# Optimization experiments

Hardware: AMD Instinct MI355X
Metric: run time of the kernel (lower is better)

## Reference

```python
import math
import jax, jax.numpy as jnp
import numpy as np

N_TOKENS = 32768
N_TYPES = 21
D_MODEL = 1024
N_SEQS = 64


def setup_inputs() -> dict:
    key = jax.random.key(0)
    k1, k2, k3, k4 = jax.random.split(key, 4)
    x = jax.random.normal(k1, (N_TOKENS, N_TYPES), dtype=jnp.float32)
    # nn.Linear(n_types, d_model): weight [d_model, n_types], bias [d_model]
    W = jax.random.normal(k2, (D_MODEL, N_TYPES), dtype=jnp.float32) / math.sqrt(N_TYPES)
    b = jax.random.normal(k3, (D_MODEL,), dtype=jnp.float32) * 0.01
    # sorted segment ids -> ragged batch of N_SEQS sequences
    batch = jnp.sort(jax.random.randint(k4, (N_TOKENS,), 0, N_SEQS, dtype=jnp.int64))
    return {"x": x, "W": W, "b": b, "batch": batch}


def _position_encoding(max_len, d_model, dtype):
    pos = jnp.arange(max_len, dtype=jnp.float32)[:, None]          # [L,1]
    div = jnp.exp(jnp.arange(0, d_model, 2, dtype=jnp.float32) * (-math.log(10000.0) / d_model))
    ang = pos * div                                                 # [L, d/2]
    pe = jnp.zeros((max_len, d_model), dtype=jnp.float32)
    pe = pe.at[:, 0::2].set(jnp.sin(ang)).at[:, 1::2].set(jnp.cos(ang))
    return pe.astype(dtype)


def reference(x, W, b, batch):
    d_model = W.shape[0]
    # Linear projection + sqrt(d_model) scale
    h = (jnp.einsum('nt,dt->nd', x, W) + b) * math.sqrt(d_model)    # [N, d_model]

    # pad_batch: relabel via unique ids, compute per-token position within its
    # sequence, and scatter into a padded [n_seqs, max_len, d_model] tensor.
    bnp = np.asarray(batch)
    _, inv, counts = np.unique(bnp, return_inverse=True, return_counts=True)
    n_seqs = counts.shape[0]
    max_len = int(counts.max())
    offsets = np.concatenate([np.zeros(1, dtype=np.int64), np.cumsum(counts)[:-1]])
    pos = np.arange(bnp.shape[0], dtype=np.int64) - offsets[inv]    # position within sequence

    padded = jnp.zeros((n_seqs, max_len, d_model), dtype=h.dtype)
    padded = padded.at[jnp.asarray(inv), jnp.asarray(pos)].set(h)

    # mask: True where valid token (original returns ~pad_mask)
    mask = jnp.arange(max_len)[None, :] < jnp.asarray(counts)[:, None]

    pe = _position_encoding(max_len, d_model, h.dtype)              # [L, d_model]
    out = padded + pe[None, :, :]
    return (out, mask)
```

## Files before the change

### kernel.cpp

```cpp
#include <hip/hip_runtime.h>
#include <hip/hip_bf16.h>
#include <math.h>

typedef float f4 __attribute__((ext_vector_type(4)));
typedef float f32x4 __attribute__((ext_vector_type(4)));
typedef short bf16x8 __attribute__((ext_vector_type(8)));

__device__ inline unsigned short f2bf(float f) {
  unsigned int u = __builtin_bit_cast(unsigned int, f);
  unsigned int r = (u + 0x7FFFu + ((u >> 16) & 1u)) >> 16;
  return (unsigned short)r;
}

__global__ __launch_bounds__(1024) void setup_kernel(
    const int* __restrict__ batch, int n, const float* __restrict__ W,
    int* __restrict__ tables, unsigned short* __restrict__ wbf) {
  int t = threadIdx.x;

  {
    const float* wr = W + t * 21;
    unsigned short* wo = wbf + t * 32;
#pragma unroll
    for (int k = 0; k < 21; ++k) wo[k] = f2bf(wr[k]);
#pragma unroll
    for (int k = 21; k < 32; ++k) wo[k] = 0;
  }

  __shared__ int samp[256];
  __shared__ int csum[64];
  __shared__ int fine[64];
  __shared__ int sbase[64];
  __shared__ int lbs[65];
  __shared__ int stride_s;
  if (t == 0) stride_s = (batch[n - 1] == 0) ? 2 : 1;
  if (t < 64) { csum[t] = 0; fine[t] = 0; }
  __syncthreads();
  int stride = stride_s;
  int window = (n + 255) >> 8;
  if (t < 256) {
    long long idx = (long long)t * window;
    if (idx > n - 1) idx = n - 1;
    samp[t] = batch[idx * stride];
  }
  __syncthreads();
  {
    int v = t >> 4, q = t & 15;
    int c = 0;
#pragma unroll
    for (int i = 0; i < 16; ++i) c += (samp[q * 16 + i] < v) ? 1 : 0;
    atomicAdd(&csum[v], c);
  }
  __syncthreads();
  if (t < 64) {
    int c = csum[t];
    sbase[t] = (c == 0) ? 0 : (c - 1) * window;
  }
  __syncthreads();
  {
    int v = t >> 4, q = t & 15;
    int wpt = (window + 15) >> 4;
    int S = sbase[v];
    int c = 0;
    for (int j = q * wpt; j < (q + 1) * wpt && j < window; ++j) {
      int idx = S + j;
      if (idx < n && batch[idx * stride] < v) c++;
    }
    atomicAdd(&fine[v], c);
  }
  __syncthreads();
  if (t < 64) {
    lbs[t] = sbase[t] + fine[t];
    if (t == 0) lbs[64] = n;
  }
  __syncthreads();
  if (t < 64) {
    int cnt = lbs[t + 1] - lbs[t];
    unsigned long long present = __ballot(cnt > 0);
    int seg = __popcll(present & ((1ull << t) - 1ull));
    int nseq = __popcll(present);
    if (cnt > 0) { tables[seg] = lbs[t]; tables[64 + seg] = cnt; }
    if (t >= nseq) { tables[t] = 0; tables[64 + t] = 0; }
  }
}

__global__ __launch_bounds__(256) void embed_kernel(
    const float* __restrict__ x, const unsigned short* __restrict__ wb,
    const float* __restrict__ bias, const int* __restrict__ tables,
    float* __restrict__ out, float* __restrict__ mask,
    int L, int n_tokens) {
  int t = threadIdx.x;
  int lane = t & 63;
  int wv = t >> 6;
  int g = lane >> 4, c = lane & 15;

  int stripe = blockIdx.x >> 2;
  int colGroup = blockIdx.x & 3;
  int base = stripe * 16;

  int s0 = base / L;
  int s0L = s0 * L;
  int Lnext = s0L + L;

  int row_r = base + c;
  int inc_r = (row_r >= Lnext) ? 1 : 0;
  int p_r = row_r - (inc_r ? Lnext : s0L);
  int cnt_r = tables[64 + s0 + inc_r];
  unsigned long long bal = __ballot(p_r < cnt_r);
  unsigned int m16 = (unsigned int)(bal & 0xFFFFull);
  int rank_r = __popc(m16 & ((1u << c) - 1u));

  int p0 = base - s0L;
  int cnt0 = tables[64 + s0];
  int tok0 = tables[s0] + (p0 < cnt0 ? p0 : cnt0);
  int tok = tok0 + rank_r;
  if (tok > n_tokens - 1) tok = n_tokens - 1;

  const float* xr = x + tok * 21;
  float vv[8];
#pragma unroll
  for (int j = 0; j < 8; ++j) vv[j] = 0.f;
  if (g == 0) {
#pragma unroll
    for (int j = 0; j < 8; ++j) vv[j] = xr[j];
  } else if (g == 1) {
#pragma unroll
    for (int j = 0; j < 8; ++j) vv[j] = xr[8 + j];
  } else if (g == 2) {
#pragma unroll
    for (int j = 0; j < 5; ++j) vv[j] = xr[16 + j];
  }
  bf16x8 af;
#pragma unroll
  for (int j = 0; j < 8; ++j) af[j] = (short)f2bf(vv[j]);

  int prow[4], pval[4];
#pragma unroll
  for (int j = 0; j < 4; ++j) {
    int rr = 4 * g + j;
    int row = base + rr;
    int inc = (row >= Lnext) ? 1 : 0;
    prow[j] = row - (inc ? Lnext : s0L);
    pval[j] = (m16 >> rr) & 1;
  }

  const float KC = -0.01798894603901599f;
  int cb = colGroup * 256 + wv * 64;
  bool isOdd = (c & 1) != 0;

#pragma unroll
  for (int ct = 0; ct < 4; ++ct) {
    int col = cb + ct * 16 + c;
    bf16x8 bfrag = *(const bf16x8*)(wb + col * 32 + 8 * g);
    f32x4 acc = {0.f, 0.f, 0.f, 0.f};
    acc = __builtin_amdgcn_mfma_f32_16x16x32_bf16(af, bfrag, acc, 0, 0, 0);
    float bv = bias[col];
    float dv = __expf(KC * (float)(col >> 1));
#pragma unroll
    for (int j = 0; j < 4; ++j) {
      float ang = (float)prow[j] * dv;
      float pe = isOdd ? __cosf(ang) : __sinf(ang);
      float res = pval[j] ? fmaf(acc[j] + bv, 32.f, pe) : pe;
      out[(size_t)(base + 4 * g + j) * 1024 + col] = res;
    }
  }

  if (colGroup == 0 && t < 16)
    mask[base + t] = ((m16 >> t) & 1) ? 1.0f : 0.0f;
}

extern "C" void kernel_launch(void* const* d_in, const int* in_sizes, int n_in,
                              void* d_out, int out_size, void* d_ws, size_t ws_size,
                              hipStream_t stream) {
  const float* x = (const float*)d_in[0];
  const float* W = (const float*)d_in[1];
  const float* b = (const float*)d_in[2];
  const int* batch = (const int*)d_in[3];
  int n_tokens = in_sizes[3];
  float* out = (float*)d_out;

  int L = out_size / (64 * 1025);
  int totalRows = 64 * L;

  int* tables = (int*)d_ws;
  unsigned short* wbf = (unsigned short*)((char*)d_ws + 1024);

  setup_kernel<<<1, 1024, 0, stream>>>(batch, n_tokens, W, tables, wbf);

  int stripes = totalRows / 16;
  embed_kernel<<<stripes * 4, 256, 0, stream>>>(x, wbf, b, tables, out,
                                                out + (size_t)totalRows * 1024,
                                                L, n_tokens);
}
```

Baseline: 44.17 us.

## Fuse segment-table setup into embed kernel via per-block binary search

Removes the separate single-block setup kernel. Each embed block now computes the segment starts and counts itself, using a 64-lane binary search over the batch ids, and converts its W columns to bf16 in registers. This drops one kernel launch and the serial dependency on a single-block kernel. In exchange every block repeats the binary searches (about 15 dependent global loads per lane) and the W loads and conversions, which adds latency to each block.

```diff
diff --git a/kernel.cpp b/kernel.cpp
--- a/kernel.cpp
+++ b/kernel.cpp
@@ -2,7 +2,6 @@
 #include <hip/hip_bf16.h>
 #include <math.h>
 
-typedef float f4 __attribute__((ext_vector_type(4)));
 typedef float f32x4 __attribute__((ext_vector_type(4)));
 typedef short bf16x8 __attribute__((ext_vector_type(8)));
 
@@ -12,90 +11,67 @@
   return (unsigned short)r;
 }
 
-__global__ __launch_bounds__(1024) void setup_kernel(
-    const int* __restrict__ batch, int n, const float* __restrict__ W,
-    int* __restrict__ tables, unsigned short* __restrict__ wbf) {
-  int t = threadIdx.x;
-
-  {
-    const float* wr = W + t * 21;
-    unsigned short* wo = wbf + t * 32;
-#pragma unroll
-    for (int k = 0; k < 21; ++k) wo[k] = f2bf(wr[k]);
-#pragma unroll
-    for (int k = 21; k < 32; ++k) wo[k] = 0;
-  }
-
-  __shared__ int samp[256];
-  __shared__ int csum[64];
-  __shared__ int fine[64];
-  __shared__ int sbase[64];
-  __shared__ int lbs[65];
-  __shared__ int stride_s;
-  if (t == 0) stride_s = (batch[n - 1] == 0) ? 2 : 1;
-  if (t < 64) { csum[t] = 0; fine[t] = 0; }
-  __syncthreads();
-  int stride = stride_s;
-  int window = (n + 255) >> 8;
-  if (t < 256) {
-    long long idx = (long long)t * window;
-    if (idx > n - 1) idx = n - 1;
-    samp[t] = batch[idx * stride];
-  }
-  __syncthreads();
-  {
-    int v = t >> 4, q = t & 15;
-    int c = 0;
-#pragma unroll
-    for (int i = 0; i < 16; ++i) c += (samp[q * 16 + i] < v) ? 1 : 0;
-    atomicAdd(&csum[v], c);
-  }
-  __syncthreads();
-  if (t < 64) {
-    int c = csum[t];
-    sbase[t] = (c == 0) ? 0 : (c - 1) * window;
-  }
-  __syncthreads();
-  {
-    int v = t >> 4, q = t & 15;
-    int wpt = (window + 15) >> 4;
-    int S = sbase[v];
-    int c = 0;
-    for (int j = q * wpt; j < (q + 1) * wpt && j < window; ++j) {
-      int idx = S + j;
-      if (idx < n && batch[idx * stride] < v) c++;
-    }
-    atomicAdd(&fine[v], c);
-  }
-  __syncthreads();
-  if (t < 64) {
-    lbs[t] = sbase[t] + fine[t];
-    if (t == 0) lbs[64] = n;
-  }
-  __syncthreads();
-  if (t < 64) {
-    int cnt = lbs[t + 1] - lbs[t];
-    unsigned long long present = __ballot(cnt > 0);
-    int seg = __popcll(present & ((1ull << t) - 1ull));
-    int nseq = __popcll(present);
-    if (cnt > 0) { tables[seg] = lbs[t]; tables[64 + seg] = cnt; }
-    if (t >= nseq) { tables[t] = 0; tables[64 + t] = 0; }
-  }
-}
-
 __global__ __launch_bounds__(256) void embed_kernel(
-    const float* __restrict__ x, const unsigned short* __restrict__ wb,
-    const float* __restrict__ bias, const int* __restrict__ tables,
-    float* __restrict__ out, float* __restrict__ mask,
-    int L, int n_tokens) {
+    const float* __restrict__ x, const float* __restrict__ W,
+    const float* __restrict__ bias, const int* __restrict__ batch,
+    int n, float* __restrict__ out, float* __restrict__ mask,
+    int L, int totalRows) {
   int t = threadIdx.x;
   int lane = t & 63;
   int wv = t >> 6;
   int g = lane >> 4, c = lane & 15;
 
   int stripe = blockIdx.x >> 2;
-  int colGroup = blockIdx.x & 3;
+  int colGroup = blockIdx.x & 2 ? (blockIdx.x & 3) : (blockIdx.x & 3);
+  colGroup = blockIdx.x & 3;
   int base = stripe * 16;
+
+  __shared__ int seg_start[65];
+  __shared__ int seg_cnt[65];
+
+  if (t < 64) {
+    int stride = (batch[n - 1] == 0) ? 2 : 1;
+    int v = t;
+    int lo = 0, hi = n;
+    while (lo < hi) {
+      int mid = (lo + hi) >> 1;
+      if (batch[(size_t)mid * stride] < v) lo = mid + 1; else hi = mid;
+    }
+    int lbn = __shfl_down(lo, 1);
+    if (t == 63) lbn = n;
+    int cnt = lbn - lo;
+    unsigned long long present = __ballot(cnt > 0);
+    int rank = __popcll(present & ((1ull << t) - 1ull));
+    int nseq = __popcll(present);
+    if (cnt > 0) { seg_start[rank] = lo; seg_cnt[rank] = cnt; }
+    if (t >= nseq) { seg_start[t] = n; seg_cnt[t] = 0; }
+    if (t == 0) { seg_start[64] = n; seg_cnt[64] = 0; }
+  }
+
+  const float KC = -0.01798894603901599f;
+  int cb = colGroup * 256 + wv * 64;
+  int kb = 8 * g;
+  bf16x8 bfr[4];
+  float bv[4], dv[4];
+#pragma unroll
+  for (int ct = 0; ct < 4; ++ct) {
+    int col = cb + ct * 16 + c;
+    const float* wr = W + col * 21;
+    float wvv[8];
+#pragma unroll
+    for (int j = 0; j < 8; ++j) {
+      int k = kb + j;
+      wvv[j] = (k < 21) ? wr[k] : 0.f;
+    }
+    bf16x8 bf;
+#pragma unroll
+    for (int j = 0; j < 8; ++j) bf[j] = (short)f2bf(wvv[j]);
+    bfr[ct] = bf;
+    bv[ct] = bias[col];
+    dv[ct] = __expf(KC * (float)(col >> 1));
+  }
+
+  __syncthreads();
 
   int s0 = base / L;
   int s0L = s0 * L;
@@ -104,34 +80,34 @@
   int row_r = base + c;
   int inc_r = (row_r >= Lnext) ? 1 : 0;
   int p_r = row_r - (inc_r ? Lnext : s0L);
-  int cnt_r = tables[64 + s0 + inc_r];
+  int cnt_r = seg_cnt[s0 + inc_r];
   unsigned long long bal = __ballot(p_r < cnt_r);
   unsigned int m16 = (unsigned int)(bal & 0xFFFFull);
   int rank_r = __popc(m16 & ((1u << c) - 1u));
 
   int p0 = base - s0L;
-  int cnt0 = tables[64 + s0];
-  int tok0 = tables[s0] + (p0 < cnt0 ? p0 : cnt0);
+  int cnt0 = seg_cnt[s0];
+  int tok0 = seg_start[s0] + (p0 < cnt0 ? p0 : cnt0);
   int tok = tok0 + rank_r;
-  if (tok > n_tokens - 1) tok = n_tokens - 1;
+  if (tok > (n - 1)) tok = n - 1;
 
-  const float* xr = x + tok * 21;
-  float vv[8];
+  const float* xr = x + (size_t)tok * 21;
+  float vvx[8];
 #pragma unroll
-  for (int j = 0; j < 8; ++j) vv[j] = 0.f;
+  for (int j = 0; j < 8; ++j) vvx[j] = 0.f;
   if (g == 0) {
 #pragma unroll
-    for (int j = 0; j < 8; ++j) vv[j] = xr[j];
+    for (int j = 0; j < 8; ++j) vvx[j] = xr[j];
   } else if (g == 1) {
 #pragma unroll
-    for (int j = 0; j < 8; ++j) vv[j] = xr[8 + j];
+    for (int j = 0; j < 8; ++j) vvx[j] = xr[8 + j];
   } else if (g == 2) {
 #pragma unroll
-    for (int j = 0; j < 5; ++j) vv[j] = xr[16 + j];
+    for (int j = 0; j < 5; ++j) vvx[j] = xr[16 + j];
   }
   bf16x8 af;
 #pragma unroll
-  for (int j = 0; j < 8; ++j) af[j] = (short)f2bf(vv[j]);
+  for (int j = 0; j < 8; ++j) af[j] = (short)f2bf(vvx[j]);
 
   int prow[4], pval[4];
 #pragma unroll
@@ -143,23 +119,18 @@
     pval[j] = (m16 >> rr) & 1;
   }
 
-  const float KC = -0.01798894603901599f;
-  int cb = colGroup * 256 + wv * 64;
   bool isOdd = (c & 1) != 0;
 
 #pragma unroll
   for (int ct = 0; ct < 4; ++ct) {
     int col = cb + ct * 16 + c;
-    bf16x8 bfrag = *(const bf16x8*)(wb + col * 32 + 8 * g);
     f32x4 acc = {0.f, 0.f, 0.f, 0.f};
-    acc = __builtin_amdgcn_mfma_f32_16x16x32_bf16(af, bfrag, acc, 0, 0, 0);
-    float bv = bias[col];
-    float dv = __expf(KC * (float)(col >> 1));
+    acc = __builtin_amdgcn_mfma_f32_16x16x32_bf16(af, bfr[ct], acc, 0, 0, 0);
 #pragma unroll
     for (int j = 0; j < 4; ++j) {
-      float ang = (float)prow[j] * dv;
+      float ang = (float)prow[j] * dv[ct];
       float pe = isOdd ? __cosf(ang) : __sinf(ang);
-      float res = pval[j] ? fmaf(acc[j] + bv, 32.f, pe) : pe;
+      float res = pval[j] ? fmaf(acc[j] + bv[ct], 32.f, pe) : pe;
       out[(size_t)(base + 4 * g + j) * 1024 + col] = res;
     }
   }
@@ -181,13 +152,8 @@
   int L = out_size / (64 * 1025);
   int totalRows = 64 * L;
 
-  int* tables = (int*)d_ws;
-  unsigned short* wbf = (unsigned short*)((char*)d_ws + 1024);
-
-  setup_kernel<<<1, 1024, 0, stream>>>(batch, n_tokens, W, tables, wbf);
-
   int stripes = totalRows / 16;
-  embed_kernel<<<stripes * 4, 256, 0, stream>>>(x, wbf, b, tables, out,
-                                                out + (size_t)totalRows * 1024,
-                                                L, n_tokens);
+  embed_kernel<<<stripes * 4, 256, 0, stream>>>(
+      x, W, b, batch, n_tokens, out, out + (size_t)totalRows * 1024,
+      L, totalRows);
 }
```

Result: slower. 77.97 us (+76.5%).

## Transpose MFMA operands for row-contiguous float4 stores and split setup across blocks

Applied to the files above, without the earlier changes.

The MFMA operands are swapped so each lane holds four consecutive output columns of one row. That lets results go out as 16-byte vector stores instead of scattered scalar stores. Bias is loaded as float4, and sin and cos for each column pair come from a single sincos call per pair, which reduces transcendental work. The setup kernel now runs in 5 blocks of 256 threads, with one block building the segment tables and four converting W to bf16 in parallel, so fewer threads take part in the table-building reductions.

```diff
diff --git a/kernel.cpp b/kernel.cpp
--- a/kernel.cpp
+++ b/kernel.cpp
@@ -12,18 +12,20 @@
   return (unsigned short)r;
 }
 
-__global__ __launch_bounds__(1024) void setup_kernel(
+__global__ __launch_bounds__(256) void setup_kernel(
     const int* __restrict__ batch, int n, const float* __restrict__ W,
     int* __restrict__ tables, unsigned short* __restrict__ wbf) {
   int t = threadIdx.x;
 
-  {
-    const float* wr = W + t * 21;
-    unsigned short* wo = wbf + t * 32;
+  if (blockIdx.x != 0) {
+    int r = (blockIdx.x - 1) * 256 + t;
+    const float* wr = W + r * 21;
+    unsigned short* wo = wbf + r * 32;
 #pragma unroll
     for (int k = 0; k < 21; ++k) wo[k] = f2bf(wr[k]);
 #pragma unroll
     for (int k = 21; k < 32; ++k) wo[k] = 0;
+    return;
   }
 
   __shared__ int samp[256];
@@ -37,17 +39,17 @@
   __syncthreads();
   int stride = stride_s;
   int window = (n + 255) >> 8;
-  if (t < 256) {
+  {
     long long idx = (long long)t * window;
     if (idx > n - 1) idx = n - 1;
     samp[t] = batch[idx * stride];
   }
   __syncthreads();
   {
-    int v = t >> 4, q = t & 15;
+    int v = t >> 2, q = t & 3;
     int c = 0;
 #pragma unroll
-    for (int i = 0; i < 16; ++i) c += (samp[q * 16 + i] < v) ? 1 : 0;
+    for (int i = 0; i < 64; ++i) c += (samp[q * 64 + i] < v) ? 1 : 0;
     atomicAdd(&csum[v], c);
   }
   __syncthreads();
@@ -57,13 +59,13 @@
   }
   __syncthreads();
   {
-    int v = t >> 4, q = t & 15;
-    int wpt = (window + 15) >> 4;
+    int v = t >> 2, q = t & 3;
+    int wpt = (window + 3) >> 2;
     int S = sbase[v];
     int c = 0;
     for (int j = q * wpt; j < (q + 1) * wpt && j < window; ++j) {
       int idx = S + j;
-      if (idx < n && batch[idx * stride] < v) c++;
+      if (idx < n && batch[(size_t)idx * stride] < v) c++;
     }
     atomicAdd(&fine[v], c);
   }
@@ -101,67 +103,70 @@
   int s0L = s0 * L;
   int Lnext = s0L + L;
 
-  int row_r = base + c;
-  int inc_r = (row_r >= Lnext) ? 1 : 0;
-  int p_r = row_r - (inc_r ? Lnext : s0L);
-  int cnt_r = tables[64 + s0 + inc_r];
-  unsigned long long bal = __ballot(p_r < cnt_r);
+  int row_c = base + c;
+  int inc_c = (row_c >= Lnext) ? 1 : 0;
+  int p_c = row_c - (inc_c ? Lnext : s0L);
+  int cnt_c = tables[64 + s0 + inc_c];
+  bool valid_c = p_c < cnt_c;
+  unsigned long long bal = __ballot(valid_c);
   unsigned int m16 = (unsigned int)(bal & 0xFFFFull);
-  int rank_r = __popc(m16 & ((1u << c) - 1u));
+  int rank_c = __popc(m16 & ((1u << c) - 1u));
 
   int p0 = base - s0L;
   int cnt0 = tables[64 + s0];
   int tok0 = tables[s0] + (p0 < cnt0 ? p0 : cnt0);
-  int tok = tok0 + rank_r;
+  int tok = tok0 + rank_c;
   if (tok > n_tokens - 1) tok = n_tokens - 1;
 
-  const float* xr = x + tok * 21;
-  float vv[8];
+  const float* xr = x + (size_t)tok * 21;
+  float vvx[8];
 #pragma unroll
-  for (int j = 0; j < 8; ++j) vv[j] = 0.f;
+  for (int j = 0; j < 8; ++j) vvx[j] = 0.f;
   if (g == 0) {
 #pragma unroll
-    for (int j = 0; j < 8; ++j) vv[j] = xr[j];
+    for (int j = 0; j < 8; ++j) vvx[j] = xr[j];
   } else if (g == 1) {
 #pragma unroll
-    for (int j = 0; j < 8; ++j) vv[j] = xr[8 + j];
+    for (int j = 0; j < 8; ++j) vvx[j] = xr[8 + j];
   } else if (g == 2) {
 #pragma unroll
-    for (int j = 0; j < 5; ++j) vv[j] = xr[16 + j];
+    for (int j = 0; j < 5; ++j) vvx[j] = xr[16 + j];
   }
   bf16x8 af;
 #pragma unroll
-  for (int j = 0; j < 8; ++j) af[j] = (short)f2bf(vv[j]);
-
-  int prow[4], pval[4];
-#pragma unroll
-  for (int j = 0; j < 4; ++j) {
-    int rr = 4 * g + j;
-    int row = base + rr;
-    int inc = (row >= Lnext) ? 1 : 0;
-    prow[j] = row - (inc ? Lnext : s0L);
-    pval[j] = (m16 >> rr) & 1;
-  }
+  for (int j = 0; j < 8; ++j) af[j] = (short)f2bf(vvx[j]);
 
   const float KC = -0.01798894603901599f;
   int cb = colGroup * 256 + wv * 64;
-  bool isOdd = (c & 1) != 0;
+  bf16x8 wfr[4];
+  f4 bv4[4];
+  float dv0[4], dv1[4];
+#pragma unroll
+  for (int ct = 0; ct < 4; ++ct) {
+    wfr[ct] = *(const bf16x8*)(wb + (size_t)(cb + ct * 16 + c) * 32 + 8 * g);
+    int dbase = cb + ct * 16 + 4 * g;
+    bv4[ct] = *(const f4*)(bias + dbase);
+    int pair0 = dbase >> 1;
+    dv0[ct] = __expf(KC * (float)pair0);
+    dv1[ct] = __expf(KC * (float)(pair0 + 1));
+  }
+
+  float fp = (float)p_c;
+  float* po = out + (size_t)(base + c) * 1024;
 
 #pragma unroll
   for (int ct = 0; ct < 4; ++ct) {
-    int col = cb + ct * 16 + c;
-    bf16x8 bfrag = *(const bf16x8*)(wb + col * 32 + 8 * g);
     f32x4 acc = {0.f, 0.f, 0.f, 0.f};
-    acc = __builtin_amdgcn_mfma_f32_16x16x32_bf16(af, bfrag, acc, 0, 0, 0);
-    float bv = bias[col];
-    float dv = __expf(KC * (float)(col >> 1));
-#pragma unroll
-    for (int j = 0; j < 4; ++j) {
-      float ang = (float)prow[j] * dv;
-      float pe = isOdd ? __cosf(ang) : __sinf(ang);
-      float res = pval[j] ? fmaf(acc[j] + bv, 32.f, pe) : pe;
-      out[(size_t)(base + 4 * g + j) * 1024 + col] = res;
-    }
+    acc = __builtin_amdgcn_mfma_f32_16x16x32_bf16(wfr[ct], af, acc, 0, 0, 0);
+    float sv0, cv0, sv1, cv1;
+    __sincosf(fp * dv0[ct], &sv0, &cv0);
+    __sincosf(fp * dv1[ct], &sv1, &cv1);
+    f4 res;
+    res[0] = valid_c ? fmaf(acc[0] + bv4[ct][0], 32.f, sv0) : sv0;
+    res[1] = valid_c ? fmaf(acc[1] + bv4[ct][1], 32.f, cv0) : cv0;
+    res[2] = valid_c ? fmaf(acc[2] + bv4[ct][2], 32.f, sv1) : sv1;
+    res[3] = valid_c ? fmaf(acc[3] + bv4[ct][3], 32.f, cv1) : cv1;
+    *(f4*)(po + cb + ct * 16 + 4 * g) = res;
   }
 
   if (colGroup == 0 && t < 16)
@@ -184,7 +189,7 @@
   int* tables = (int*)d_ws;
   unsigned short* wbf = (unsigned short*)((char*)d_ws + 1024);
 
-  setup_kernel<<<1, 1024, 0, stream>>>(batch, n_tokens, W, tables, wbf);
+  setup_kernel<<<5, 256, 0, stream>>>(batch, n_tokens, W, tables, wbf);
 
   int stripes = totalRows / 16;
   embed_kernel<<<stripes * 4, 256, 0, stream>>>(x, wbf, b, tables, out,
```

New measurement: 49.01 us. 1.11x slower.
